# Performance work log

Measured on AMD Instinct MI355X. Metric: run time of the kernel, lower is better.

The kernel has to match this reference:

```python
import jax, jax.numpy as jnp
import numpy as np

K1 = 3                      # spline kernel size per pseudo dim
SIZE = float(np.sqrt(2.0))  # pseudo_cartesian normalization size


def spline_weights(p, k):
    """Degree-1 open B-spline basis over 2D pseudo coords.
    p: [..., 2] in [0,1]. Returns basis [..., 4], weight_index [..., 4]."""
    v = jnp.clip(p, 0.0, 1.0) * (k - 1)
    lo = jnp.floor(v)
    frac = v - lo
    lo = lo.astype(jnp.int32)
    off = jnp.array([0, 1], dtype=jnp.int32)
    w0 = jnp.stack([1.0 - frac[..., 0], frac[..., 0]], axis=-1)   # [...,2]
    w1 = jnp.stack([1.0 - frac[..., 1], frac[..., 1]], axis=-1)   # [...,2]
    i0 = jnp.clip(lo[..., 0:1] + off, 0, k - 1)                    # [...,2]
    i1 = jnp.clip(lo[..., 1:2] + off, 0, k - 1)                    # [...,2]
    basis = (w0[..., :, None] * w1[..., None, :]).reshape(*p.shape[:-1], 4)
    widx = (i0[..., :, None] + k * i1[..., None, :]).reshape(*p.shape[:-1], 4)
    return basis, widx


def setup_inputs() -> dict:
    key = jax.random.key(0)
    kx, ke, kp, kq, kw, kb = jax.random.split(key, 6)
    N, C, P, E, K = 50000, 64, 16, 800000, K1 * K1
    x = jax.random.normal(kx, (N, C), dtype=jnp.float32)
    pos = jax.random.uniform(kp, (N, 2), dtype=jnp.float32)
    pose = jax.random.normal(kq, (N, P, 2), dtype=jnp.float32)
    pose = pose / (jnp.linalg.norm(pose, axis=-1, keepdims=True) + 1e-8)  # unit pose vectors
    W = jax.random.normal(kw, (P, K, C), dtype=jnp.float32) / np.sqrt(C * 4.0)
    bias = jax.random.normal(kb, (P,), dtype=jnp.float32) * 0.01
    edge_index = jax.random.randint(ke, (2, E), 0, N, dtype=jnp.int64)
    return {"x": x, "pos": pos, "pose": pose, "W": W, "bias": bias,
            "edge_index": edge_index}


def reference(x, pos, pose, W, bias, edge_index):
    N, C = x.shape
    P = pose.shape[1]
    row, col = edge_index[0], edge_index[1]
    # pseudo_cartesian: normalized relative position in [0,1]^2
    pseudo = (pos[col] - pos[row]) / (2.0 * SIZE) + 0.5              # [E,2]
    # posevec_to_rotmat on detached pose vectors
    pose_c = jax.lax.stop_gradient(pose)
    a, b = pose_c[..., 0], pose_c[..., 1]
    R = jnp.stack([jnp.stack([a, -b], -1), jnp.stack([b, a], -1)], -2)  # [N,P,2,2]
    Re = R[row]                                                      # [E,P,2,2]
    # rotate pseudo coords about (0.5, 0.5), batched over all poses
    p = jnp.einsum('epij,ej->epi', Re, pseudo - 0.5) + 0.5           # [E,P,2]
    basis, widx = spline_weights(p, K1)                              # [E,P,4]
    # SplineConv (out_channels=1, no root weight, no norm):
    # precompute per-node per-pose per-kernel-bin projections
    Z = jnp.einsum('nc,pkc->npk', x, W)                              # [N,P,K]
    pidx = jnp.arange(P)[None, :, None]
    vals = Z[col[:, None, None], pidx, widx]                         # [E,P,4]
    msg = jnp.sum(basis * vals, axis=-1)                             # [E,P]
    out = jax.ops.segment_sum(msg, row, num_segments=N)              # [N,P]
    return out + bias[None, :]
```

## Files before the change

### kernel.cpp

```cpp
#include <hip/hip_runtime.h>
#include <hip/hip_bf16.h>

#define C_DIM 64
#define P_DIM 16
#define K_DIM 9
#define PK (P_DIM * K_DIM)
#define INV2S 0.35355339059327373f

__global__ __launch_bounds__(256) void init_out_kernel(float* __restrict__ out,
                                                       const float* __restrict__ bias,
                                                       int total) {
    int i = blockIdx.x * 256 + threadIdx.x;
    if (i < total) out[i] = bias[i & (P_DIM - 1)];
}

__global__ __launch_bounds__(256) void z_gemm_kernel(const float* __restrict__ x,
                                                     const float* __restrict__ W,
                                                     __hip_bfloat16* __restrict__ Zb,
                                                     int N) {
    __shared__ float xs[C_DIM][C_DIM + 4];

    const int block_row = blockIdx.x * 64;

    for (int i = threadIdx.x; i < C_DIM * (C_DIM / 4); i += 256) {
        int r = i >> 4, c4 = i & 15;
        int gr = block_row + r;
        float4 v = make_float4(0.0f, 0.0f, 0.0f, 0.0f);
        if (gr < N) v = ((const float4*)x)[(size_t)gr * (C_DIM / 4) + c4];
        *(float4*)&xs[r][c4 * 4] = v;
    }
    __syncthreads();

    const int rg = threadIdx.x & 15;
    const int p  = threadIdx.x >> 4;
    const int j0 = p * K_DIM;

    float acc[4][K_DIM];
    #pragma unroll
    for (int i = 0; i < 4; ++i)
        #pragma unroll
        for (int k = 0; k < K_DIM; ++k) acc[i][k] = 0.0f;

    const float4* W4 = (const float4*)W;
    #pragma unroll 4
    for (int cs = 0; cs < 16; ++cs) {
        float4 xv[4];
        #pragma unroll
        for (int i = 0; i < 4; ++i) xv[i] = *(const float4*)&xs[rg + 16 * i][cs * 4];
        #pragma unroll
        for (int k = 0; k < K_DIM; ++k) {
            float4 wv = W4[(size_t)(j0 + k) * (C_DIM / 4) + cs];
            #pragma unroll
            for (int i = 0; i < 4; ++i) {
                acc[i][k] = fmaf(xv[i].x, wv.x, acc[i][k]);
                acc[i][k] = fmaf(xv[i].y, wv.y, acc[i][k]);
                acc[i][k] = fmaf(xv[i].z, wv.z, acc[i][k]);
                acc[i][k] = fmaf(xv[i].w, wv.w, acc[i][k]);
            }
        }
    }

    #pragma unroll
    for (int i = 0; i < 4; ++i) {
        int gr = block_row + rg + 16 * i;
        if (gr < N) {
            __hip_bfloat16* zp = Zb + (size_t)gr * PK + j0;
            #pragma unroll
            for (int k = 0; k < K_DIM; ++k) zp[k] = __float2bfloat16(acc[i][k]);
        }
    }
}

__global__ __launch_bounds__(256) void edge_kernel(const int* __restrict__ ei,
                                                   const float* __restrict__ pos,
                                                   const float* __restrict__ pose,
                                                   const __hip_bfloat16* __restrict__ Zb,
                                                   float* __restrict__ out,
                                                   int E) {
    const int p  = threadIdx.x & 15;
    const int eg = threadIdx.x >> 4;
    const int e0 = blockIdx.x * 64 + eg;

    int  r[4], c[4];
    bool valid[4];
    #pragma unroll
    for (int it = 0; it < 4; ++it) {
        int e = e0 + it * 16;
        valid[it] = (e < E);
        int ec = valid[it] ? e : 0;
        r[it] = ei[ec];
        c[it] = ei[E + ec];
    }

    float d0[4], d1[4];
    #pragma unroll
    for (int it = 0; it < 4; ++it) {
        d0[it] = (pos[2 * c[it]]     - pos[2 * r[it]])     * INV2S;
        d1[it] = (pos[2 * c[it] + 1] - pos[2 * r[it] + 1]) * INV2S;
    }

    float2 ab[4];
    #pragma unroll
    for (int it = 0; it < 4; ++it)
        ab[it] = ((const float2*)pose)[(size_t)r[it] * P_DIM + p];

    #pragma unroll
    for (int it = 0; it < 4; ++it) {
        const float p0 = fmaf(ab[it].x, d0[it], fmaf(-ab[it].y, d1[it], 0.5f));
        const float p1 = fmaf(ab[it].y, d0[it], fmaf( ab[it].x, d1[it], 0.5f));

        const float v0 = fminf(fmaxf(p0, 0.0f), 1.0f) * 2.0f;
        const float v1 = fminf(fmaxf(p1, 0.0f), 1.0f) * 2.0f;
        const float lo0 = floorf(v0);
        const float lo1 = floorf(v1);
        const float f0 = v0 - lo0;
        const float f1 = v1 - lo1;
        const int i00 = min((int)lo0, 2);
        const int i01 = min((int)lo0 + 1, 2);
        const int i10 = min((int)lo1, 2);
        const int i11 = min((int)lo1 + 1, 2);

        const __hip_bfloat16* __restrict__ Zp = Zb + (size_t)c[it] * PK + p * K_DIM;
        const float w00 = (1.0f - f0) * (1.0f - f1);
        const float w01 = (1.0f - f0) * f1;
        const float w10 = f0 * (1.0f - f1);
        const float w11 = f0 * f1;

        float m = w00 * __bfloat162float(Zp[i00 + 3 * i10]);
        m = fmaf(w01, __bfloat162float(Zp[i00 + 3 * i11]), m);
        m = fmaf(w10, __bfloat162float(Zp[i01 + 3 * i10]), m);
        m = fmaf(w11, __bfloat162float(Zp[i01 + 3 * i11]), m);

        if (valid[it]) atomicAdd(&out[(size_t)r[it] * P_DIM + p], m);
    }
}

extern "C" void kernel_launch(void* const* d_in, const int* in_sizes, int n_in,
                              void* d_out, int out_size, void* d_ws, size_t ws_size,
                              hipStream_t stream) {
    const float* x    = (const float*)d_in[0];
    const float* pos  = (const float*)d_in[1];
    const float* pose = (const float*)d_in[2];
    const float* W    = (const float*)d_in[3];
    const float* bias = (const float*)d_in[4];
    const int*   ei   = (const int*)d_in[5];

    const int N = in_sizes[0] / C_DIM;
    const int E = in_sizes[5] / 2;

    float* out = (float*)d_out;
    __hip_bfloat16* Zb = (__hip_bfloat16*)d_ws;

    init_out_kernel<<<(N * P_DIM + 255) / 256, 256, 0, stream>>>(out, bias, N * P_DIM);
    z_gemm_kernel<<<(N + 63) / 64, 256, 0, stream>>>(x, W, Zb, N);
    edge_kernel<<<(E + 63) / 64, 256, 0, stream>>>(ei, pos, pose, Zb, out, E);
}
```

Baseline: 158.6 us.

## Fuse bias init into GEMM, stage Z via LDS, raise edge ILP

```diff
diff --git a/kernel.cpp b/kernel.cpp
--- a/kernel.cpp
+++ b/kernel.cpp
@@ -7,22 +7,29 @@
 #define PK (P_DIM * K_DIM)
 #define INV2S 0.35355339059327373f
 
-__global__ __launch_bounds__(256) void init_out_kernel(float* __restrict__ out,
-                                                       const float* __restrict__ bias,
-                                                       int total) {
-    int i = blockIdx.x * 256 + threadIdx.x;
-    if (i < total) out[i] = bias[i & (P_DIM - 1)];
-}
+#define ZS_STRIDE 152
+#define SH_FLOATS 4864
 
 __global__ __launch_bounds__(256) void z_gemm_kernel(const float* __restrict__ x,
                                                      const float* __restrict__ W,
+                                                     const float* __restrict__ bias,
+                                                     float* __restrict__ out,
                                                      __hip_bfloat16* __restrict__ Zb,
                                                      int N) {
-    __shared__ float xs[C_DIM][C_DIM + 4];
+    __shared__ float sh_raw[SH_FLOATS];
+    float (*xs)[C_DIM + 4] = (float(*)[C_DIM + 4])sh_raw;
+    __hip_bfloat16* zs = (__hip_bfloat16*)sh_raw;
 
     const int block_row = blockIdx.x * 64;
+    const int tid = threadIdx.x;
 
-    for (int i = threadIdx.x; i < C_DIM * (C_DIM / 4); i += 256) {
+    {
+        const float4 b4 = ((const float4*)bias)[tid & 3];
+        const int o4 = block_row * 4 + tid;
+        if (o4 < N * 4) ((float4*)out)[o4] = b4;
+    }
+
+    for (int i = tid; i < C_DIM * (C_DIM / 4); i += 256) {
         int r = i >> 4, c4 = i & 15;
         int gr = block_row + r;
         float4 v = make_float4(0.0f, 0.0f, 0.0f, 0.0f);
@@ -31,8 +38,8 @@
     }
     __syncthreads();
 
-    const int rg = threadIdx.x & 15;
-    const int p  = threadIdx.x >> 4;
+    const int rg = tid & 15;
+    const int p  = tid >> 4;
     const int j0 = p * K_DIM;
 
     float acc[4][K_DIM];
@@ -59,18 +66,27 @@
             }
         }
     }
+    __syncthreads();
 
     #pragma unroll
     for (int i = 0; i < 4; ++i) {
-        int gr = block_row + rg + 16 * i;
-        if (gr < N) {
-            __hip_bfloat16* zp = Zb + (size_t)gr * PK + j0;
-            #pragma unroll
-            for (int k = 0; k < K_DIM; ++k) zp[k] = __float2bfloat16(acc[i][k]);
-        }
+        __hip_bfloat16* zrow = &zs[(rg + 16 * i) * ZS_STRIDE + j0];
+        #pragma unroll
+        for (int k = 0; k < K_DIM; ++k)
+            zrow[k] = __float2bfloat16(acc[i][k]);
+    }
+    __syncthreads();
+
+    const int nrow = min(64, N - block_row);
+    float4* Zb4 = (float4*)Zb;
+    for (int i = tid; i < nrow * 18; i += 256) {
+        int row = i / 18, q = i - row * 18;
+        float4 v = *(const float4*)&zs[row * ZS_STRIDE + q * 8];
+        Zb4[(size_t)(block_row + row) * 18 + q] = v;
     }
 }
 
+#define EILP 8
 __global__ __launch_bounds__(256) void edge_kernel(const int* __restrict__ ei,
                                                    const float* __restrict__ pos,
                                                    const float* __restrict__ pose,
@@ -79,12 +95,12 @@
                                                    int E) {
     const int p  = threadIdx.x & 15;
     const int eg = threadIdx.x >> 4;
-    const int e0 = blockIdx.x * 64 + eg;
+    const int e0 = blockIdx.x * (16 * EILP) + eg;
 
-    int  r[4], c[4];
-    bool valid[4];
+    int  r[EILP], c[EILP];
+    bool valid[EILP];
     #pragma unroll
-    for (int it = 0; it < 4; ++it) {
+    for (int it = 0; it < EILP; ++it) {
         int e = e0 + it * 16;
         valid[it] = (e < E);
         int ec = valid[it] ? e : 0;
@@ -92,20 +108,22 @@
         c[it] = ei[E + ec];
     }
 
-    float d0[4], d1[4];
+    float d0[EILP], d1[EILP];
     #pragma unroll
-    for (int it = 0; it < 4; ++it) {
-        d0[it] = (pos[2 * c[it]]     - pos[2 * r[it]])     * INV2S;
-        d1[it] = (pos[2 * c[it] + 1] - pos[2 * r[it] + 1]) * INV2S;
+    for (int it = 0; it < EILP; ++it) {
+        const float2 pc = ((const float2*)pos)[c[it]];
+        const float2 pr = ((const float2*)pos)[r[it]];
+        d0[it] = (pc.x - pr.x) * INV2S;
+        d1[it] = (pc.y - pr.y) * INV2S;
     }
 
-    float2 ab[4];
+    float2 ab[EILP];
     #pragma unroll
-    for (int it = 0; it < 4; ++it)
+    for (int it = 0; it < EILP; ++it)
         ab[it] = ((const float2*)pose)[(size_t)r[it] * P_DIM + p];
 
     #pragma unroll
-    for (int it = 0; it < 4; ++it) {
+    for (int it = 0; it < EILP; ++it) {
         const float p0 = fmaf(ab[it].x, d0[it], fmaf(-ab[it].y, d1[it], 0.5f));
         const float p1 = fmaf(ab[it].y, d0[it], fmaf( ab[it].x, d1[it], 0.5f));
 
@@ -151,7 +169,6 @@
     float* out = (float*)d_out;
     __hip_bfloat16* Zb = (__hip_bfloat16*)d_ws;
 
-    init_out_kernel<<<(N * P_DIM + 255) / 256, 256, 0, stream>>>(out, bias, N * P_DIM);
-    z_gemm_kernel<<<(N + 63) / 64, 256, 0, stream>>>(x, W, Zb, N);
-    edge_kernel<<<(E + 63) / 64, 256, 0, stream>>>(ei, pos, pose, Zb, out, E);
+    z_gemm_kernel<<<(N + 63) / 64, 256, 0, stream>>>(x, W, bias, out, Zb, N);
+    edge_kernel<<<(E + 16 * EILP - 1) / (16 * EILP), 256, 0, stream>>>(ei, pos, pose, Zb, out, E);
 }
```

Result: no change. 156.3 us (-1.4%).
